# Kernel tuning notes

Measured on AMD Instinct MI355X. Metric: run time of the kernel, lower is better.

## Reference

```python
import jax, jax.numpy as jnp
import numpy as np

B, S, E, H, W = 4, 2048, 1024, 16, 128
HD = E // H

def setup_inputs() -> dict:
    key = jax.random.key(0)
    ks = jax.random.split(key, 5)
    scale = 1.0 / np.sqrt(E)
    x = jax.random.normal(ks[0], (B, S, E), dtype=jnp.float32)
    w_in = jax.random.uniform(ks[1], (3 * E, E), dtype=jnp.float32, minval=-scale, maxval=scale)
    b_in = jnp.zeros((3 * E,), dtype=jnp.float32)
    w_out = jax.random.uniform(ks[2], (E, E), dtype=jnp.float32, minval=-scale, maxval=scale)
    b_out = jnp.zeros((E,), dtype=jnp.float32)
    return {"x": x, "w_in": w_in, "b_in": b_in, "w_out": w_out, "b_out": b_out}

def reference(x, w_in, b_in, w_out, b_out):
    b, s, e = x.shape
    # fused QKV projection (torch MultiheadAttention in_proj)
    qkv = x @ w_in.T + b_in                      # [B,S,3E]
    q, k, v = jnp.split(qkv, 3, axis=-1)
    q = q.reshape(b, s, H, HD).transpose(0, 2, 1, 3)  # [B,H,S,HD]
    k = k.reshape(b, s, H, HD).transpose(0, 2, 1, 3)
    v = v.reshape(b, s, H, HD).transpose(0, 2, 1, 3)
    scores = jnp.einsum('bhqd,bhkd->bhqk', q, k) / jnp.sqrt(jnp.asarray(HD, x.dtype))
    # banded causal mask: row i attends to columns [i-W, i]
    i = jnp.arange(s)[:, None]
    j = jnp.arange(s)[None, :]
    allowed = (j <= i) & (j >= i - W)            # [S,S]
    scores = jnp.where(allowed[None, None], scores, jnp.asarray(-1e9, x.dtype))
    attn = jax.nn.softmax(scores, axis=-1)
    out = jnp.einsum('bhqk,bhkd->bhqd', attn, v)  # [B,H,S,HD]
    out = out.transpose(0, 2, 1, 3).reshape(b, s, e)
    return out @ w_out.T + b_out
```

## Files before the change

kernel.cpp:

```cpp
#include <hip/hip_runtime.h>
#include <stdint.h>

#define SLEN 2048
#define EMB  1024
#define NHEAD 16
#define HDIM  64
#define WINSZ 128

typedef __attribute__((ext_vector_type(8))) __bf16 bf16x8;
typedef __attribute__((ext_vector_type(4))) float  f32x4;

__device__ __forceinline__ unsigned short f2bf(float f) {
  union { float f; unsigned int u; } v;
  v.f = f;
  unsigned int r = v.u + 0x7FFFu + ((v.u >> 16) & 1u);
  return (unsigned short)(r >> 16);
}

__device__ __forceinline__ unsigned int pack_bf(float a, float b) {
  union { float f; unsigned int u; } x, y;
  x.f = a; y.f = b;
  return ((y.u + 0x8000u) & 0xFFFF0000u) | ((x.u + 0x8000u) >> 16);
}

__global__ void cvt_all(const float* __restrict__ x,
                        const float* __restrict__ wi,
                        const float* __restrict__ wo,
                        unsigned short* __restrict__ dst) {
  const long n0 = 8388608, n1 = n0 + 3145728, n2 = n1 + 1048576;
  long i = ((long)blockIdx.x * 256 + threadIdx.x) * 4;
  if (i >= n2) return;
  const float* src; long off;
  if (i < n0)      { src = x;  off = i; }
  else if (i < n1) { src = wi; off = i - n0; }
  else             { src = wo; off = i - n1; }
  float4 f = *(const float4*)(src + off);
  ushort4 o;
  o.x = f2bf(f.x); o.y = f2bf(f.y); o.z = f2bf(f.z); o.w = f2bf(f.w);
  *(ushort4*)(dst + i) = o;
}

#define AS1(p) (const __attribute__((address_space(1))) unsigned int*)((const void*)(p))
#define AS3(p) (__attribute__((address_space(3))) unsigned int*)((void*)(p))

template <int MODE>
__global__ __launch_bounds__(256, 2) void gemm_nt(
    const unsigned short* __restrict__ A,
    const unsigned short* __restrict__ B,
    const float* __restrict__ bias,
    void* __restrict__ Cout,
    unsigned short* __restrict__ vt,
    int M, int N, int K, int ldc)
{
  __shared__ unsigned short As[128 * 64];
  __shared__ unsigned short Bs[128 * 64];
  const int tid  = threadIdx.x;
  const int wave = tid >> 6, lane = tid & 63;
  const int quad = lane >> 4, l16 = lane & 15;
  const int wm = (wave >> 1) * 64, wn = (wave & 1) * 64;
  const long mBase = (long)blockIdx.y * 128;
  const long nBase = (long)blockIdx.x * 128;
  const int lr  = lane >> 3;
  const int lks = ((lane & 7) ^ lr) * 8;
  const int swz = l16 & 7;

  f32x4 acc[4][4];
#pragma unroll
  for (int i = 0; i < 4; ++i)
#pragma unroll
    for (int j = 0; j < 4; ++j)
#pragma unroll
      for (int r = 0; r < 4; ++r) acc[i][j][r] = 0.f;

  for (int k0 = 0; k0 < K; k0 += 64) {
    __syncthreads();
#pragma unroll
    for (int t = 0; t < 4; ++t) {
      const int r0 = (wave * 4 + t) * 8;
      const unsigned short* ga = A + (mBase + r0 + lr) * (long)K + k0 + lks;
      __builtin_amdgcn_global_load_lds(AS1(ga), AS3(As + r0 * 64), 16, 0, 0);
      const unsigned short* gb = B + (nBase + r0 + lr) * (long)K + k0 + lks;
      __builtin_amdgcn_global_load_lds(AS1(gb), AS3(Bs + r0 * 64), 16, 0, 0);
    }
    __syncthreads();

#pragma unroll
    for (int s = 0; s < 2; ++s) {
      bf16x8 aF[4], bF[4];
#pragma unroll
      for (int i = 0; i < 4; ++i)
        aF[i] = *(const bf16x8*)(As + (wm + i * 16 + l16) * 64 + (((s * 4 + quad) ^ swz) * 8));
#pragma unroll
      for (int j = 0; j < 4; ++j)
        bF[j] = *(const bf16x8*)(Bs + (wn + j * 16 + l16) * 64 + (((s * 4 + quad) ^ swz) * 8));
#pragma unroll
      for (int i = 0; i < 4; ++i)
#pragma unroll
        for (int j = 0; j < 4; ++j)
          acc[i][j] = __builtin_amdgcn_mfma_f32_16x16x32_bf16(aF[i], bF[j], acc[i][j], 0, 0, 0);
    }
  }

  if (MODE == 1 && nBase >= 2048) {
#pragma unroll
    for (int j = 0; j < 4; ++j) {
      const int nG = (int)nBase + wn + j * 16 + l16;
      const float bv = bias[nG];
      const int hd = nG - 2048;
      const int hh = hd >> 6, dd = hd & 63;
#pragma unroll
      for (int i = 0; i < 4; ++i) {
        const int mG0 = (int)mBase + wm + i * 16 + quad * 4;
        const int bb = mG0 >> 11, ss = mG0 & 2047;
        ushort4 o;
        o.x = f2bf(acc[i][j][0] + bv);
        o.y = f2bf(acc[i][j][1] + bv);
        o.z = f2bf(acc[i][j][2] + bv);
        o.w = f2bf(acc[i][j][3] + bv);
        *(ushort4*)(vt + (((long)(bb * NHEAD + hh)) * HDIM + dd) * SLEN + ss) = o;
      }
    }
  } else {
#pragma unroll
    for (int j = 0; j < 4; ++j) {
      const long nG = nBase + wn + j * 16 + l16;
      const float bv = bias[nG];
#pragma unroll
      for (int i = 0; i < 4; ++i)
#pragma unroll
        for (int r = 0; r < 4; ++r) {
          const long mG = mBase + wm + i * 16 + quad * 4 + r;
          const float v = acc[i][j][r] + bv;
          if (MODE == 1) ((unsigned short*)Cout)[mG * ldc + nG] = f2bf(v);
          else           ((float*)Cout)[mG * ldc + nG] = v;
        }
    }
  }
}

__global__ __launch_bounds__(512, 4) void local_attn(
    const unsigned short* __restrict__ qk,
    const unsigned short* __restrict__ vT,
    unsigned short* __restrict__ outw)
{
  const int qb = blockIdx.x;
  const int h  = blockIdx.y;
  const int b  = blockIdx.z;
  const int tid = threadIdx.x;
  const int wave = tid >> 6, lane = tid & 63;
  const int quad = lane >> 4, l16 = lane & 15;

  __shared__ unsigned short Klds[256 * 64];
  __shared__ unsigned short Vlds[64 * 256];

  const int kwin0 = qb * 128 - WINSZ;

  {
    const int kr = lane >> 3, kc = lane & 7;
    const long colOff = 1024 + h * HDIM + ((kc ^ kr) * 8);
#pragma unroll
    for (int t = 0; t < 4; ++t) {
      const int u = wave * 4 + t;
      const int sk = max(kwin0 + u * 8 + kr, 0);
      const unsigned short* g = qk + (long)(b * SLEN + sk) * 2048 + colOff;
      __builtin_amdgcn_global_load_lds(AS1(g), AS3(Klds + u * 512), 16, 0, 0);
    }
  }
  {
    const unsigned short* vbase = vT + ((long)(b * NHEAD + h)) * HDIM * SLEN;
#pragma unroll
    for (int t = 0; t < 4; ++t) {
      const int c = t * 512 + tid;
      const int d = c >> 5, k8 = c & 31;
      const int s0 = max(kwin0 + k8 * 8, 0);
      uint4 v = *(const uint4*)(vbase + (long)d * SLEN + s0);
      *(uint4*)(Vlds + d * 256 + ((k8 ^ (d & 7)) * 8)) = v;
    }
  }

  const int q0 = qb * 128 + wave * 16;
  const long qrow = (long)(b * SLEN + q0 + l16) * 2048 + h * HDIM;
  const bf16x8 qB0 = *(const bf16x8*)(qk + qrow + quad * 8);
  const bf16x8 qB1 = *(const bf16x8*)(qk + qrow + 32 + quad * 8);

  __syncthreads();

  const int lbase = (wave * 16) & ~31;
  const int kx = l16 & 7;
  const int a0 = (quad ^ kx) * 8;
  const int a1 = ((4 + quad) ^ kx) * 8;
  f32x4 sc[5][2];
#pragma unroll
  for (int it = 0; it < 5; ++it) {
    const int l0 = lbase + it * 32;
#pragma unroll
    for (int half = 0; half < 2; ++half) {
      const unsigned short* kr_ = Klds + (l0 + half * 16 + l16) * 64;
      const bf16x8 kA0 = *(const bf16x8*)(kr_ + a0);
      const bf16x8 kA1 = *(const bf16x8*)(kr_ + a1);
      f32x4 s;
#pragma unroll
      for (int r = 0; r < 4; ++r) s[r] = 0.f;
      s = __builtin_amdgcn_mfma_f32_16x16x32_bf16(kA0, qB0, s, 0, 0, 0);
      s = __builtin_amdgcn_mfma_f32_16x16x32_bf16(kA1, qB1, s, 0, 0, 0);
      sc[it][half] = s;
    }
  }

  const int qlocal = WINSZ + wave * 16 + l16;
  const int lo = max(wave * 16 + l16, kwin0 < 0 ? -kwin0 : 0);
  const int kb = lbase + quad * 4;
  float m = -3.0e38f;
#pragma unroll
  for (int it = 0; it < 5; ++it)
#pragma unroll
    for (int half = 0; half < 2; ++half)
#pragma unroll
      for (int r = 0; r < 4; ++r) {
        const int kl = kb + it * 32 + half * 16 + r;
        float v = sc[it][half][r] * 0.125f;
        v = (kl >= lo && kl <= qlocal) ? v : -3.0e38f;
        sc[it][half][r] = v;
        m = fmaxf(m, v);
      }
  m = fmaxf(m, __shfl_xor(m, 16, 64));
  m = fmaxf(m, __shfl_xor(m, 32, 64));

  float lsum = 0.f;
#pragma unroll
  for (int it = 0; it < 5; ++it)
#pragma unroll
    for (int half = 0; half < 2; ++half)
#pragma unroll
      for (int r = 0; r < 4; ++r) {
        const float e = __expf(sc[it][half][r] - m);
        sc[it][half][r] = e;
        lsum += e;
      }
  lsum += __shfl_xor(lsum, 16, 64);
  lsum += __shfl_xor(lsum, 32, 64);
  const float invl = 1.0f / lsum;

  f32x4 Oacc[4];
#pragma unroll
  for (int dt = 0; dt < 4; ++dt)
#pragma unroll
    for (int r = 0; r < 4; ++r) Oacc[dt][r] = 0.f;

#pragma unroll
  for (int it = 0; it < 5; ++it) {
    const int l0 = lbase + it * 32;
    const unsigned int u0 = pack_bf(sc[it][0][0], sc[it][0][1]);
    const unsigned int u1 = pack_bf(sc[it][0][2], sc[it][0][3]);
    const unsigned int u2 = pack_bf(sc[it][1][0], sc[it][1][1]);
    const unsigned int u3 = pack_bf(sc[it][1][2], sc[it][1][3]);
    unsigned int breg[4];
#pragma unroll
    for (int r = 0; r < 4; ++r) {
      const int srcl = ((quad & 1) * 2 + (r >> 1)) * 16 + l16;
      const unsigned int ga = __shfl((int)((r & 1) ? u1 : u0), srcl, 64);
      const unsigned int gb = __shfl((int)((r & 1) ? u3 : u2), srcl, 64);
      breg[r] = (quad >> 1) ? gb : ga;
    }
    union { unsigned int u[4]; bf16x8 v; } pB;
    pB.u[0] = breg[0]; pB.u[1] = breg[1]; pB.u[2] = breg[2]; pB.u[3] = breg[3];

    const int chBase = (l0 >> 3);
#pragma unroll
    for (int dt = 0; dt < 4; ++dt) {
      const int ch = (chBase + quad) ^ kx;
      const bf16x8 vA = *(const bf16x8*)(Vlds + (dt * 16 + l16) * 256 + ch * 8);
      Oacc[dt] = __builtin_amdgcn_mfma_f32_16x16x32_bf16(vA, pB.v, Oacc[dt], 0, 0, 0);
    }
  }

  const long obase = (long)(b * SLEN + q0 + l16) * EMB + h * HDIM;
#pragma unroll
  for (int dt = 0; dt < 4; ++dt) {
    ushort4 o;
    o.x = f2bf(Oacc[dt][0] * invl);
    o.y = f2bf(Oacc[dt][1] * invl);
    o.z = f2bf(Oacc[dt][2] * invl);
    o.w = f2bf(Oacc[dt][3] * invl);
    *(ushort4*)(outw + obase + dt * 16 + quad * 4) = o;
  }
}

extern "C" void kernel_launch(void* const* d_in, const int* in_sizes, int n_in,
                              void* d_out, int out_size, void* d_ws, size_t ws_size,
                              hipStream_t stream) {
  const float* x     = (const float*)d_in[0];
  const float* w_in  = (const float*)d_in[1];
  const float* b_in  = (const float*)d_in[2];
  const float* w_out = (const float*)d_in[3];
  const float* b_out = (const float*)d_in[4];
  float* out = (float*)d_out;

  char* ws = (char*)d_ws;
  unsigned short* xb    = (unsigned short*)(ws + 0);
  unsigned short* winb  = (unsigned short*)(ws + 16777216);
  unsigned short* woutb = (unsigned short*)(ws + 23068672);
  unsigned short* qkb   = (unsigned short*)(ws + 25165824);
  unsigned short* attn  = (unsigned short*)(ws + 58720256);
  unsigned short* vT    = (unsigned short*)(ws + 75497472);

  const long ncv = 8388608 + 3145728 + 1048576;
  cvt_all<<<(int)(ncv / 1024), 256, 0, stream>>>(x, w_in, w_out, xb);

  gemm_nt<1><<<dim3(3072 / 128, 8192 / 128), 256, 0, stream>>>(
      xb, winb, b_in, (void*)qkb, vT, 8192, 3072, 1024, 2048);

  local_attn<<<dim3(SLEN / 128, NHEAD, 4), 512, 0, stream>>>(qkb, vT, attn);

  gemm_nt<0><<<dim3(1024 / 128, 8192 / 128), 256, 0, stream>>>(
      attn, woutb, b_out, (void*)out, nullptr, 8192, 1024, 1024, 1024);
}
```

Baseline: 199.5 us.

## Double-buffer GEMM K-tiles with 128x256 blocks, 8 waves, and XCD-aware block swizzle

Reworks the bf16 NT GEMM to use 128x256 output tiles computed by 8 waves of 512 threads. K-tiles are staged in two 32-wide halves across a double-buffered LDS region, and prefetches are issued with explicit vmcnt waits and barriers so global loads overlap the MFMA work. It also remaps block indices so consecutive tiles are spread across chiplets, and raises wave priority around the MFMA bursts. The intent is to hide global-load latency and raise compute density. In exchange, the LDS layout loses its XOR swizzle, which can cause bank conflicts, the LDS footprint grows to 96KB, and the hand-set wait counts make correctness fragile.

```diff
diff --git a/kernel.cpp b/kernel.cpp
--- a/kernel.cpp
+++ b/kernel.cpp
@@ -44,7 +44,7 @@
 #define AS3(p) (__attribute__((address_space(3))) unsigned int*)((void*)(p))
 
 template <int MODE>
-__global__ __launch_bounds__(256, 2) void gemm_nt(
+__global__ __launch_bounds__(512, 2) void gemm_nt(
     const unsigned short* __restrict__ A,
     const unsigned short* __restrict__ B,
     const float* __restrict__ bias,
@@ -52,17 +52,35 @@
     unsigned short* __restrict__ vt,
     int M, int N, int K, int ldc)
 {
-  __shared__ unsigned short As[128 * 64];
-  __shared__ unsigned short Bs[128 * 64];
+  __shared__ unsigned short lds[49152];
   const int tid  = threadIdx.x;
   const int wave = tid >> 6, lane = tid & 63;
   const int quad = lane >> 4, l16 = lane & 15;
-  const int wm = (wave >> 1) * 64, wn = (wave & 1) * 64;
-  const long mBase = (long)blockIdx.y * 128;
-  const long nBase = (long)blockIdx.x * 128;
-  const int lr  = lane >> 3;
-  const int lks = ((lane & 7) ^ lr) * 8;
-  const int swz = l16 & 7;
+  const int wm = (wave >> 2) * 64, wn = (wave & 3) * 64;
+
+  const int nwgx = gridDim.x;
+  const int nwg  = nwgx * gridDim.y;
+  const int orig = blockIdx.y * nwgx + blockIdx.x;
+  const int swz  = (orig & 7) * (nwg >> 3) + (orig >> 3);
+  const long mBase = (long)(swz / nwgx) * 128;
+  const long nBase = (long)(swz % nwgx) * 256;
+
+  const int srow = lane >> 2, scol = (lane & 3) * 8;
+  const unsigned short* Abase = A + (mBase + wave * 16 + srow) * (long)K + scol;
+  const unsigned short* Bb0   = B + (nBase + (wave * 2 + 0) * 16 + srow) * (long)K + scol;
+  const unsigned short* Bb1   = B + (nBase + (wave * 2 + 1) * 16 + srow) * (long)K + scol;
+  const int aLd  = wave * 512;
+  const int bLd0 = (wave * 2 + 0) * 512, bLd1 = (wave * 2 + 1) * 512;
+
+#define AREG(b, kh) (lds + ((b) * 2 + (kh)) * 4096)
+#define BREG(b, kh) (lds + 16384 + ((b) * 2 + (kh)) * 8192)
+#define STAGE(TT, KH) do {                                                           \
+    const int _b = (TT) & 1;                                                         \
+    const long _kc = (long)(TT) * 64 + (KH) * 32;                                    \
+    __builtin_amdgcn_global_load_lds(AS1(Abase + _kc), AS3(AREG(_b, KH) + aLd), 16, 0, 0);  \
+    __builtin_amdgcn_global_load_lds(AS1(Bb0 + _kc),   AS3(BREG(_b, KH) + bLd0), 16, 0, 0); \
+    __builtin_amdgcn_global_load_lds(AS1(Bb1 + _kc),   AS3(BREG(_b, KH) + bLd1), 16, 0, 0); \
+  } while (0)
 
   f32x4 acc[4][4];
 #pragma unroll
@@ -72,34 +90,74 @@
 #pragma unroll
       for (int r = 0; r < 4; ++r) acc[i][j][r] = 0.f;
 
-  for (int k0 = 0; k0 < K; k0 += 64) {
-    __syncthreads();
-#pragma unroll
-    for (int t = 0; t < 4; ++t) {
-      const int r0 = (wave * 4 + t) * 8;
-      const unsigned short* ga = A + (mBase + r0 + lr) * (long)K + k0 + lks;
-      __builtin_amdgcn_global_load_lds(AS1(ga), AS3(As + r0 * 64), 16, 0, 0);
-      const unsigned short* gb = B + (nBase + r0 + lr) * (long)K + k0 + lks;
-      __builtin_amdgcn_global_load_lds(AS1(gb), AS3(Bs + r0 * 64), 16, 0, 0);
-    }
-    __syncthreads();
-
-#pragma unroll
-    for (int s = 0; s < 2; ++s) {
+  const int NT = K >> 6;
+
+  STAGE(0, 0); STAGE(0, 1); STAGE(1, 0);
+  asm volatile("s_waitcnt vmcnt(6)" ::: "memory");
+  __builtin_amdgcn_s_barrier();
+
+  for (int T = 0; T < NT; ++T) {
+    const int buf = T & 1;
+    {
+      const unsigned short* Ar = AREG(buf, 0);
+      const unsigned short* Br = BREG(buf, 0);
       bf16x8 aF[4], bF[4];
 #pragma unroll
       for (int i = 0; i < 4; ++i)
-        aF[i] = *(const bf16x8*)(As + (wm + i * 16 + l16) * 64 + (((s * 4 + quad) ^ swz) * 8));
+        aF[i] = *(const bf16x8*)(Ar + (wm + i * 16 + l16) * 32 + quad * 8);
 #pragma unroll
       for (int j = 0; j < 4; ++j)
-        bF[j] = *(const bf16x8*)(Bs + (wn + j * 16 + l16) * 64 + (((s * 4 + quad) ^ swz) * 8));
+        bF[j] = *(const bf16x8*)(Br + (wn + j * 16 + l16) * 32 + quad * 8);
+      if (T + 1 < NT) {
+        STAGE(T + 1, 1);
+        asm volatile("s_waitcnt vmcnt(6)" ::: "memory");
+      } else {
+        asm volatile("s_waitcnt vmcnt(0)" ::: "memory");
+      }
+      __builtin_amdgcn_s_barrier();
+      asm volatile("s_waitcnt lgkmcnt(0)" ::: "memory");
+      __builtin_amdgcn_sched_barrier(0);
+      __builtin_amdgcn_s_setprio(1);
 #pragma unroll
       for (int i = 0; i < 4; ++i)
 #pragma unroll
         for (int j = 0; j < 4; ++j)
           acc[i][j] = __builtin_amdgcn_mfma_f32_16x16x32_bf16(aF[i], bF[j], acc[i][j], 0, 0, 0);
-    }
-  }
+      __builtin_amdgcn_s_setprio(0);
+      __builtin_amdgcn_s_barrier();
+    }
+    {
+      const unsigned short* Ar = AREG(buf, 1);
+      const unsigned short* Br = BREG(buf, 1);
+      bf16x8 aF[4], bF[4];
+#pragma unroll
+      for (int i = 0; i < 4; ++i)
+        aF[i] = *(const bf16x8*)(Ar + (wm + i * 16 + l16) * 32 + quad * 8);
+#pragma unroll
+      for (int j = 0; j < 4; ++j)
+        bF[j] = *(const bf16x8*)(Br + (wn + j * 16 + l16) * 32 + quad * 8);
+      if (T + 2 < NT) {
+        STAGE(T + 2, 0);
+        asm volatile("s_waitcnt vmcnt(6)" ::: "memory");
+      } else if (T + 1 < NT) {
+        asm volatile("s_waitcnt vmcnt(3)" ::: "memory");
+      }
+      __builtin_amdgcn_s_barrier();
+      asm volatile("s_waitcnt lgkmcnt(0)" ::: "memory");
+      __builtin_amdgcn_sched_barrier(0);
+      __builtin_amdgcn_s_setprio(1);
+#pragma unroll
+      for (int i = 0; i < 4; ++i)
+#pragma unroll
+        for (int j = 0; j < 4; ++j)
+          acc[i][j] = __builtin_amdgcn_mfma_f32_16x16x32_bf16(aF[i], bF[j], acc[i][j], 0, 0, 0);
+      __builtin_amdgcn_s_setprio(0);
+      __builtin_amdgcn_s_barrier();
+    }
+  }
+#undef STAGE
+#undef AREG
+#undef BREG
 
   if (MODE == 1 && nBase >= 2048) {
 #pragma unroll
@@ -307,11 +365,11 @@
   const long ncv = 8388608 + 3145728 + 1048576;
   cvt_all<<<(int)(ncv / 1024), 256, 0, stream>>>(x, w_in, w_out, xb);
 
-  gemm_nt<1><<<dim3(3072 / 128, 8192 / 128), 256, 0, stream>>>(
+  gemm_nt<1><<<dim3(3072 / 256, 8192 / 128), 512, 0, stream>>>(
       xb, winb, b_in, (void*)qkb, vT, 8192, 3072, 1024, 2048);
 
   local_attn<<<dim3(SLEN / 128, NHEAD, 4), 512, 0, stream>>>(qkb, vT, attn);
 
-  gemm_nt<0><<<dim3(1024 / 128, 8192 / 128), 256, 0, stream>>>(
+  gemm_nt<0><<<dim3(1024 / 256, 8192 / 128), 512, 0, stream>>>(
       attn, woutb, b_out, (void*)out, nullptr, 8192, 1024, 1024, 1024);
 }
```

New measurement: 218.9 us. +9.7%, slower.

## Triple-buffer GEMM loads with 128x256 tiles, 8 waves, and block swizzle

Applied to the files above, without the earlier changes.

The bf16 GEMM moves from a 128x128 tile with 4 waves to a 128x256 tile with 8 waves. It replaces the two-barrier single-buffer loop with a three-stage LDS ring buffer, where global-to-LDS loads for tile T+2 are issued while MFMAs run on tile T. The loop uses explicit vmcnt waits, a single barrier per iteration, and setprio around the MFMA burst. It also remaps block indices in groups of 8 for better L2 locality. The cost is a 144KB LDS footprint, which likely allows only one block per CU.

```diff
diff --git a/kernel.cpp b/kernel.cpp
--- a/kernel.cpp
+++ b/kernel.cpp
@@ -44,7 +44,7 @@
 #define AS3(p) (__attribute__((address_space(3))) unsigned int*)((void*)(p))
 
 template <int MODE>
-__global__ __launch_bounds__(256, 2) void gemm_nt(
+__global__ __launch_bounds__(512, 2) void gemm_nt(
     const unsigned short* __restrict__ A,
     const unsigned short* __restrict__ B,
     const float* __restrict__ bias,
@@ -52,17 +52,36 @@
     unsigned short* __restrict__ vt,
     int M, int N, int K, int ldc)
 {
-  __shared__ unsigned short As[128 * 64];
-  __shared__ unsigned short Bs[128 * 64];
+  __shared__ unsigned short lds[73728];
   const int tid  = threadIdx.x;
   const int wave = tid >> 6, lane = tid & 63;
   const int quad = lane >> 4, l16 = lane & 15;
-  const int wm = (wave >> 1) * 64, wn = (wave & 1) * 64;
-  const long mBase = (long)blockIdx.y * 128;
-  const long nBase = (long)blockIdx.x * 128;
+  const int wm = (wave >> 2) * 64, wn = (wave & 3) * 64;
+  const int swz = l16 & 7;
+
+  const int nwgx = gridDim.x;
+  const int nwg  = nwgx * gridDim.y;
+  const int orig = blockIdx.y * nwgx + blockIdx.x;
+  const int bswz = (orig & 7) * (nwg >> 3) + (orig >> 3);
+  const long mBase = (long)(bswz / nwgx) * 128;
+  const long nBase = (long)(bswz % nwgx) * 256;
+
   const int lr  = lane >> 3;
   const int lks = ((lane & 7) ^ lr) * 8;
-  const int swz = l16 & 7;
+  const unsigned short* Abase = A + (mBase + lr) * (long)K + lks;
+  const unsigned short* Bbase = B + (nBase + lr) * (long)K + lks;
+
+#define STAGE3(TT, dstOff, H) do {                                                     \
+    const long _kc = (long)(TT) * 64;                                                  \
+    const int _ar = wave * 16 + (H) * 8;                                               \
+    const int _br = wave * 32 + (H) * 16;                                              \
+    __builtin_amdgcn_global_load_lds(AS1(Abase + (long)_ar * K + _kc),                 \
+                                     AS3(lds + (dstOff) + _ar * 64), 16, 0, 0);        \
+    __builtin_amdgcn_global_load_lds(AS1(Bbase + (long)_br * K + _kc),                 \
+                                     AS3(lds + (dstOff) + 8192 + _br * 64), 16, 0, 0); \
+    __builtin_amdgcn_global_load_lds(AS1(Bbase + (long)(_br + 8) * K + _kc),           \
+                                     AS3(lds + (dstOff) + 8192 + (_br + 8) * 64), 16, 0, 0); \
+  } while (0)
 
   f32x4 acc[4][4];
 #pragma unroll
@@ -72,34 +91,46 @@
 #pragma unroll
       for (int r = 0; r < 4; ++r) acc[i][j][r] = 0.f;
 
-  for (int k0 = 0; k0 < K; k0 += 64) {
-    __syncthreads();
-#pragma unroll
-    for (int t = 0; t < 4; ++t) {
-      const int r0 = (wave * 4 + t) * 8;
-      const unsigned short* ga = A + (mBase + r0 + lr) * (long)K + k0 + lks;
-      __builtin_amdgcn_global_load_lds(AS1(ga), AS3(As + r0 * 64), 16, 0, 0);
-      const unsigned short* gb = B + (nBase + r0 + lr) * (long)K + k0 + lks;
-      __builtin_amdgcn_global_load_lds(AS1(gb), AS3(Bs + r0 * 64), 16, 0, 0);
-    }
-    __syncthreads();
+  const int NT = K >> 6;
+
+  STAGE3(0, 0, 0); STAGE3(0, 0, 1);
+  STAGE3(1, 24576, 0); STAGE3(1, 24576, 1);
+
+  int curOff = 0, stgOff = 49152;
+  for (int T = 0; T < NT; ++T) {
+    if (T + 1 < NT) asm volatile("s_waitcnt vmcnt(6)" ::: "memory");
+    else            asm volatile("s_waitcnt vmcnt(0)" ::: "memory");
+    __builtin_amdgcn_s_barrier();
+    __builtin_amdgcn_sched_barrier(0);
+
+    const unsigned short* Ar = lds + curOff;
+    const unsigned short* Br = lds + curOff + 8192;
+    const bool doStage = (T + 2 < NT);
 
 #pragma unroll
     for (int s = 0; s < 2; ++s) {
       bf16x8 aF[4], bF[4];
 #pragma unroll
       for (int i = 0; i < 4; ++i)
-        aF[i] = *(const bf16x8*)(As + (wm + i * 16 + l16) * 64 + (((s * 4 + quad) ^ swz) * 8));
+        aF[i] = *(const bf16x8*)(Ar + (wm + i * 16 + l16) * 64 + (((s * 4 + quad) ^ swz) * 8));
 #pragma unroll
       for (int j = 0; j < 4; ++j)
-        bF[j] = *(const bf16x8*)(Bs + (wn + j * 16 + l16) * 64 + (((s * 4 + quad) ^ swz) * 8));
+        bF[j] = *(const bf16x8*)(Br + (wn + j * 16 + l16) * 64 + (((s * 4 + quad) ^ swz) * 8));
+      if (doStage) STAGE3(T + 2, stgOff, s);
+      asm volatile("s_waitcnt lgkmcnt(0)" ::: "memory");
+      __builtin_amdgcn_sched_barrier(0);
+      __builtin_amdgcn_s_setprio(1);
 #pragma unroll
       for (int i = 0; i < 4; ++i)
 #pragma unroll
         for (int j = 0; j < 4; ++j)
           acc[i][j] = __builtin_amdgcn_mfma_f32_16x16x32_bf16(aF[i], bF[j], acc[i][j], 0, 0, 0);
-    }
-  }
+      __builtin_amdgcn_s_setprio(0);
+    }
+    curOff = (curOff == 49152) ? 0 : curOff + 24576;
+    stgOff = (stgOff == 49152) ? 0 : stgOff + 24576;
+  }
+#undef STAGE3
 
   if (MODE == 1 && nBase >= 2048) {
 #pragma unroll
@@ -307,11 +338,11 @@
   const long ncv = 8388608 + 3145728 + 1048576;
   cvt_all<<<(int)(ncv / 1024), 256, 0, stream>>>(x, w_in, w_out, xb);
 
-  gemm_nt<1><<<dim3(3072 / 128, 8192 / 128), 256, 0, stream>>>(
+  gemm_nt<1><<<dim3(3072 / 256, 8192 / 128), 512, 0, stream>>>(
       xb, winb, b_in, (void*)qkb, vT, 8192, 3072, 1024, 2048);
 
   local_attn<<<dim3(SLEN / 128, NHEAD, 4), 512, 0, stream>>>(qkb, vT, attn);
 
-  gemm_nt<0><<<dim3(1024 / 128, 8192 / 128), 256, 0, stream>>>(
+  gemm_nt<0><<<dim3(1024 / 256, 8192 / 128), 512, 0, stream>>>(
       attn, woutb, b_out, (void*)out, nullptr, 8192, 1024, 1024, 1024);
 }
```

Result: no change. 203.3 us (+1.9%).
